# Performance work log

Measured on AMD Instinct MI355X. Metric: run time of the kernel, lower is better.

Reference implementation:

```python
import jax, jax.numpy as jnp
import numpy as np

B, S, D = 4, 8192, 512
WS = 512        # window_size
LB = 1          # look_backward (look_forward = 0, causal)


def setup_inputs() -> dict:
    key = jax.random.key(0)
    k1, k2, k3 = jax.random.split(key, 3)
    text = jax.random.normal(k1, (B, S, D), dtype=jnp.float32)
    audio = jax.random.normal(k2, (B, S, D), dtype=jnp.float32)
    video = jax.random.normal(k3, (B, S, D), dtype=jnp.float32)
    return {"text": text, "audio": audio, "video": video}


def _local_attention(q, k, v, ws=WS, lb=LB):
    # q, k, v: [b, n, d]; sliding-window causal attention, each query window
    # attends to its own window plus `lb` previous windows.
    b, n, d = q.shape
    w = n // ws
    scale = d ** -0.5
    qw = q.reshape(b, w, ws, d) * scale
    kw = k.reshape(b, w, ws, d)
    vw = v.reshape(b, w, ws, d)

    def look_around(x):
        # pad lb windows of zeros at the front, gather lb+1 shifted views
        padded = jnp.pad(x, ((0, 0), (lb, 0), (0, 0), (0, 0)))
        return jnp.concatenate([padded[:, i:i + w] for i in range(lb + 1)], axis=2)

    kk = look_around(kw)  # [b, w, (lb+1)*ws, d]
    vv = look_around(vw)

    # absolute positions for causal + padding mask
    t = jnp.arange(n).reshape(w, ws)                        # query positions [w, ws]
    tk = jnp.pad(t, ((lb, 0), (0, 0)), constant_values=-1)  # pad windows get -1
    bq_k = jnp.concatenate([tk[i:i + w] for i in range(lb + 1)], axis=1)  # [w, (lb+1)*ws]
    mask = (t[:, :, None] >= bq_k[:, None, :]) & (bq_k[:, None, :] >= 0)  # [w, ws, (lb+1)*ws]

    sim = jnp.einsum('bwid,bwjd->bwij', qw, kk)             # [b, w, ws, (lb+1)*ws]
    sim = jnp.where(mask[None], sim, jnp.finfo(sim.dtype).min)
    attn = jax.nn.softmax(sim, axis=-1)
    out = jnp.einsum('bwij,bwjd->bwid', attn, vv)
    return out.reshape(b, n, d)


def reference(text, audio, video):
    # GATSBlock.forward: x = self.local_attn(text, audio, video)
    # i.e. q = text, k = audio, v = video (modalities pre-projected to [b, n, d])
    return _local_attention(text, audio, video)
```

## Files before the change

### kernel.cpp

```cpp
#include <hip/hip_runtime.h>
#include <hip/hip_bf16.h>

#define S_ 8192
#define D_ 512
#define WSZ 512
#define QBLK 128
#define KBLK 32
#define ATT_THREADS 512
#define ATT_LDS (2 * 65536)

using bf16x8 = __attribute__((ext_vector_type(8))) __bf16;
using f32x4  = __attribute__((ext_vector_type(4))) float;

#define GLDS(gp, lp) __builtin_amdgcn_global_load_lds( \
    (const __attribute__((address_space(1))) void*)(gp), \
    (__attribute__((address_space(3))) void*)(lp), 16, 0, 0)

__global__ __launch_bounds__(256) void cvt_k(const float* __restrict__ in,
                                             ushort* __restrict__ out) {
    const int bid = blockIdx.x;
    const int j = bid & 7, t = (bid >> 3) & 255, b = bid >> 11;
    const int u = j * 256 + threadIdx.x;
    const int c = u >> 7, row = (u >> 2) & 31, h = u & 3;
    const float* src = in + ((size_t)(b * S_ + t * 32 + row)) * D_ + c * 32 + h * 8;
    float4 a0 = *(const float4*)(src);
    float4 a1 = *(const float4*)(src + 4);
    bf16x8 o;
    o[0] = (__bf16)a0.x; o[1] = (__bf16)a0.y; o[2] = (__bf16)a0.z; o[3] = (__bf16)a0.w;
    o[4] = (__bf16)a1.x; o[5] = (__bf16)a1.y; o[6] = (__bf16)a1.z; o[7] = (__bf16)a1.w;
    *(bf16x8*)(out + (size_t)(b * 256 + t) * 16384 + u * 8) = o;
}

__global__ __launch_bounds__(256) void tr_v(const float* __restrict__ V,
                                            char* __restrict__ Vt) {
    __shared__ float tile[64][68];
    const int bid = blockIdx.x;
    const int d0 = (bid & 7) * 64;
    const int s0 = ((bid >> 3) & 127) * 64;
    const int b  = bid >> 10;
    const int t  = threadIdx.x;
    {
        const int sl = t >> 2, cg = (t & 3) * 16;
        const float* src = V + ((size_t)b * S_ + s0 + sl) * D_ + d0 + cg;
        #pragma unroll
        for (int j = 0; j < 4; ++j) {
            float4 a = *(const float4*)(src + j * 4);
            *(float4*)&tile[sl][cg + j * 4] = a;
        }
    }
    __syncthreads();
    {
        const int dl = t >> 2, sg = (t & 3) * 16;
        const int d  = d0 + dl;
        const int tt = (s0 + sg) >> 5;
        const int h  = ((s0 + sg) & 31) >> 3;
        bf16x8 o0, o1;
        #pragma unroll
        for (int j = 0; j < 8; ++j) {
            o0[j] = (__bf16)tile[sg + j][dl];
            o1[j] = (__bf16)tile[sg + 8 + j][dl];
        }
        const size_t base = (size_t)(b * 256 + tt) * 32768 +
                            (d >> 4) * 1024 + (d & 15) * 64;
        *(bf16x8*)(Vt + base + h * 16)       = o0;
        *(bf16x8*)(Vt + base + (h + 1) * 16) = o1;
    }
}

__global__ __launch_bounds__(ATT_THREADS, 2) void gats_attn(
    const float* __restrict__ Qg, const char* __restrict__ Kbg,
    const char* __restrict__ Vtg, float* __restrict__ Og)
{
    extern __shared__ char smem[];
    const int tid  = threadIdx.x;
    const int lane = tid & 63;
    const int wv   = tid >> 6;
    const int h    = lane >> 4;
    const int lq   = lane & 15;
    const int laneK = lq * 64 + h * 16;

    const int bid = blockIdx.x;
    const int r2  = bid >> 3;
    const int w   = (bid & 7) * 2 + (r2 & 1);
    const int b   = (r2 >> 1) & 3;
    const int y   = r2 >> 3;
    const int qbase  = w * WSZ + y * QBLK;
    const int wqbase = qbase + wv * 16;

    const float* Qp  = Qg  + (size_t)b * S_ * D_;
    const char*  Kbp = Kbg + (size_t)b * 256 * 32768;
    const char*  Vtp = Vtg + (size_t)b * 256 * 32768;
    float*       Op  = Og  + (size_t)b * S_ * D_;

    const float scale = 0.044194173824159216f;
    const float L2E   = 1.44269504088896f;

    bf16x8 qf[16];
    {
        const int qrow = wqbase + lq;
        const float* qsrc = Qp + (size_t)qrow * D_ + h * 8;
        #pragma unroll
        for (int c = 0; c < 16; ++c) {
            float4 a0 = *(const float4*)(qsrc + c * 32);
            float4 a1 = *(const float4*)(qsrc + c * 32 + 4);
            bf16x8 q;
            q[0] = (__bf16)(a0.x * scale); q[1] = (__bf16)(a0.y * scale);
            q[2] = (__bf16)(a0.z * scale); q[3] = (__bf16)(a0.w * scale);
            q[4] = (__bf16)(a1.x * scale); q[5] = (__bf16)(a1.y * scale);
            q[6] = (__bf16)(a1.z * scale); q[7] = (__bf16)(a1.w * scale);
            qf[c] = q;
        }
    }

    f32x4 acc[32];
    #pragma unroll
    for (int i = 0; i < 32; ++i) acc[i] = (f32x4){0.f, 0.f, 0.f, 0.f};
    float m_run = -1e30f, l_run = 0.f;

    const int kstart = (w == 0) ? 0 : (w - 1) * WSZ;
    const int ktend  = qbase + QBLK;

    auto STAGE = [&](int bufi, int kt) {
        char* kb = smem + bufi * 65536;
        char* vb = kb + 32768;
        const size_t tb = ((size_t)(kt >> 5)) << 15;
        const char* ksrc = Kbp + tb;
        const char* vsrc = Vtp + tb;
        #pragma unroll
        for (int s2 = 0; s2 < 4; ++s2) {
            const int off = wv * 4096 + s2 * 1024;
            GLDS(ksrc + off + lane * 16, kb + off);
            GLDS(vsrc + off + lane * 16, vb + off);
        }
    };

    STAGE(0, kstart);
    int cur = 0;
    for (int kt = kstart; kt < ktend; kt += KBLK) {
        const bool hasnext = (kt + KBLK) < ktend;
        if (hasnext) {
            STAGE(cur ^ 1, kt + KBLK);
            asm volatile("s_waitcnt vmcnt(8)" ::: "memory");
        } else {
            asm volatile("s_waitcnt vmcnt(0)" ::: "memory");
        }
        __builtin_amdgcn_s_barrier();

        if (kt <= wqbase + 15) {
            char* Ksh = smem + cur * 65536;
            char* Vsh = Ksh + 32768;

            f32x4 st[2];
            __builtin_amdgcn_s_setprio(1);
            #pragma unroll
            for (int g = 0; g < 2; ++g) {
                f32x4 sa = (f32x4){0.f, 0.f, 0.f, 0.f};
                f32x4 sb = (f32x4){0.f, 0.f, 0.f, 0.f};
                #pragma unroll
                for (int c = 0; c < 16; ++c) {
                    const int byte = c * 2048 + g * 1024 + laneK;
                    bf16x8 kf = *(const bf16x8*)(Ksh + byte);
                    if (c & 1) sb = __builtin_amdgcn_mfma_f32_16x16x32_bf16(kf, qf[c], sb, 0, 0, 0);
                    else       sa = __builtin_amdgcn_mfma_f32_16x16x32_bf16(kf, qf[c], sa, 0, 0, 0);
                }
                st[g] = sa + sb;
            }
            __builtin_amdgcn_s_setprio(0);

            const int qg = wqbase + lq;
            if (kt + 31 > wqbase) {
                #pragma unroll
                for (int g = 0; g < 2; ++g)
                    #pragma unroll
                    for (int r = 0; r < 4; ++r) {
                        const int key = kt + g * 16 + h * 4 + r;
                        if (key > qg) st[g][r] = -1e30f;
                    }
            }

            float own = st[0][0];
            #pragma unroll
            for (int r = 1; r < 4; ++r) own = fmaxf(own, st[0][r]);
            #pragma unroll
            for (int r = 0; r < 4; ++r) own = fmaxf(own, st[1][r]);
            float tmax = fmaxf(own, __shfl_xor(own, 16));
            tmax = fmaxf(tmax, __shfl_xor(tmax, 32));

            if (__any(tmax > m_run + 8.f)) {
                const float mnew = fmaxf(m_run, tmax);
                const float f = exp2f((m_run - mnew) * L2E);
                m_run = mnew;
                l_run *= f;
                float fr[4];
                #pragma unroll
                for (int r = 0; r < 4; ++r) fr[r] = __shfl(f, h * 4 + r);
                #pragma unroll
                for (int dc = 0; dc < 32; ++dc)
                    #pragma unroll
                    for (int r = 0; r < 4; ++r) acc[dc][r] *= fr[r];
            }

            float p[2][4];
            float rs = 0.f;
            #pragma unroll
            for (int g = 0; g < 2; ++g)
                #pragma unroll
                for (int r = 0; r < 4; ++r) {
                    const float v = exp2f((st[g][r] - m_run) * L2E);
                    p[g][r] = v;
                    rs += v;
                }
            rs += __shfl_xor(rs, 16);
            rs += __shfl_xor(rs, 32);
            l_run += rs;

            uint c0, c1, c2, c3;
            asm("v_cvt_pk_bf16_f32 %0, %1, %2" : "=v"(c0) : "v"(p[0][0]), "v"(p[0][1]));
            asm("v_cvt_pk_bf16_f32 %0, %1, %2" : "=v"(c1) : "v"(p[0][2]), "v"(p[0][3]));
            asm("v_cvt_pk_bf16_f32 %0, %1, %2" : "=v"(c2) : "v"(p[1][0]), "v"(p[1][1]));
            asm("v_cvt_pk_bf16_f32 %0, %1, %2" : "=v"(c3) : "v"(p[1][2]), "v"(p[1][3]));
            const uint x16_0 = __shfl_xor((int)c0, 16), x16_1 = __shfl_xor((int)c1, 16);
            const uint x16_2 = __shfl_xor((int)c2, 16), x16_3 = __shfl_xor((int)c3, 16);
            const uint x32_0 = __shfl_xor((int)c0, 32), x32_1 = __shfl_xor((int)c1, 32);
            const uint x32_2 = __shfl_xor((int)c2, 32), x32_3 = __shfl_xor((int)c3, 32);
            const uint x48_0 = __shfl_xor((int)c0, 48), x48_1 = __shfl_xor((int)c1, 48);
            const uint x48_2 = __shfl_xor((int)c2, 48), x48_3 = __shfl_xor((int)c3, 48);
            union { uint u[4]; bf16x8 v; } pu;
            pu.u[0] = (h == 0) ? c0 : (h == 1) ? x48_0 : (h == 2) ? x32_2 : x16_2;
            pu.u[1] = (h == 0) ? c1 : (h == 1) ? x48_1 : (h == 2) ? x32_3 : x16_3;
            pu.u[2] = (h == 0) ? x16_0 : (h == 1) ? x32_0 : (h == 2) ? x48_2 : c2;
            pu.u[3] = (h == 0) ? x16_1 : (h == 1) ? x32_1 : (h == 2) ? x48_3 : c3;
            const bf16x8 pa = pu.v;

            __builtin_amdgcn_s_setprio(1);
            #pragma unroll
            for (int dc = 0; dc < 32; ++dc) {
                bf16x8 vf = *(const bf16x8*)(Vsh + dc * 1024 + laneK);
                acc[dc] = __builtin_amdgcn_mfma_f32_16x16x32_bf16(pa, vf, acc[dc], 0, 0, 0);
            }
            __builtin_amdgcn_s_setprio(0);
        }
        __builtin_amdgcn_s_barrier();
        cur ^= 1;
    }

    const float invq = 1.0f / l_run;
    float inv[4];
    #pragma unroll
    for (int r = 0; r < 4; ++r) inv[r] = __shfl(invq, h * 4 + r);
    #pragma unroll
    for (int dc = 0; dc < 32; ++dc) {
        #pragma unroll
        for (int r = 0; r < 4; ++r) {
            const int row = wqbase + h * 4 + r;
            const int col = dc * 16 + lq;
            Op[(size_t)row * D_ + col] = acc[dc][r] * inv[r];
        }
    }
}

#define FB_LDS (32768 + 32768 + 4 * 1024)
__global__ __launch_bounds__(256, 2) void gats_attn_fb(
    const float* __restrict__ Qg, const float* __restrict__ Kg,
    const float* __restrict__ Vg, float* __restrict__ Og)
{
    extern __shared__ char smem[];
    char* Ksh = smem;
    char* Vsh = smem + 32768;
    const int tid  = threadIdx.x;
    const int lane = tid & 63;
    const int wv   = tid >> 6;
    char* Psh = smem + 65536 + wv * 1024;
    const int bid = blockIdx.x;
    const int wh  = bid & 7;
    const int r2  = bid >> 3;
    const int w   = wh * 2 + (r2 & 1);
    const int b   = (r2 >> 1) & 3;
    const int y   = r2 >> 3;
    const int qbase  = w * WSZ + y * 64;
    const int wqbase = qbase + wv * 16;
    const size_t boff = (size_t)b * S_ * D_;
    const float* Qp = Qg + boff; const float* Kp = Kg + boff;
    const float* Vp = Vg + boff; float* Op = Og + boff;
    const float scale = 0.044194173824159216f;
    const float L2E   = 1.44269504088896f;
    bf16x8 qf[16];
    {
        const int qrow = wqbase + (lane & 15);
        const float* qsrc = Qp + (size_t)qrow * D_ + ((lane >> 4) * 8);
        #pragma unroll
        for (int c = 0; c < 16; ++c) {
            float4 a0 = *(const float4*)(qsrc + c * 32);
            float4 a1 = *(const float4*)(qsrc + c * 32 + 4);
            bf16x8 q;
            q[0] = (__bf16)(a0.x * scale); q[1] = (__bf16)(a0.y * scale);
            q[2] = (__bf16)(a0.z * scale); q[3] = (__bf16)(a0.w * scale);
            q[4] = (__bf16)(a1.x * scale); q[5] = (__bf16)(a1.y * scale);
            q[6] = (__bf16)(a1.z * scale); q[7] = (__bf16)(a1.w * scale);
            qf[c] = q;
        }
    }
    f32x4 acc[32];
    #pragma unroll
    for (int i = 0; i < 32; ++i) acc[i] = (f32x4){0.f, 0.f, 0.f, 0.f};
    float m_r[4], l_r[4];
    #pragma unroll
    for (int r = 0; r < 4; ++r) { m_r[r] = -1e30f; l_r[r] = 0.f; }
    const int kstart = (w == 0) ? 0 : (w - 1) * WSZ;
    const int ktend  = qbase + 64;
    for (int kt = kstart; kt < ktend; kt += 32) {
        __syncthreads();
        #pragma unroll
        for (int s = 0; s < 8; ++s) {
            const int row = s * 4 + wv;
            const int dof = lane * 8;
            const float4* src = (const float4*)(Kp + (size_t)(kt + row) * D_ + dof);
            float4 a0 = src[0], a1 = src[1];
            bf16x8 kv;
            kv[0] = (__bf16)a0.x; kv[1] = (__bf16)a0.y; kv[2] = (__bf16)a0.z; kv[3] = (__bf16)a0.w;
            kv[4] = (__bf16)a1.x; kv[5] = (__bf16)a1.y; kv[6] = (__bf16)a1.z; kv[7] = (__bf16)a1.w;
            const int byte = row * 1024 + ((dof * 2) ^ ((row & 7) << 4));
            *(bf16x8*)(Ksh + byte) = kv;
        }
        #pragma unroll
        for (int hh = 0; hh < 2; ++hh) {
            const int d = tid + hh * 256;
            #pragma unroll
            for (int it = 0; it < 4; ++it) {
                float vvv[8];
                #pragma unroll
                for (int j = 0; j < 8; ++j)
                    vvv[j] = Vp[(size_t)(kt + it * 8 + j) * D_ + d];
                bf16x8 vb;
                #pragma unroll
                for (int j = 0; j < 8; ++j) vb[j] = (__bf16)vvv[j];
                const int byte = d * 64 + ((it * 16) ^ (((d >> 1) & 3) << 4));
                *(bf16x8*)(Vsh + byte) = vb;
            }
        }
        __syncthreads();
        if (kt > wqbase + 15) continue;
        f32x4 sacc[2];
        #pragma unroll
        for (int g = 0; g < 2; ++g) {
            f32x4 s = (f32x4){0.f, 0.f, 0.f, 0.f};
            const int keyrow = g * 16 + (lane & 15);
            #pragma unroll
            for (int c = 0; c < 16; ++c) {
                const int byte = keyrow * 1024 +
                                 ((c * 64 + (lane >> 4) * 16) ^ ((keyrow & 7) << 4));
                bf16x8 kf = *(const bf16x8*)(Ksh + byte);
                s = __builtin_amdgcn_mfma_f32_16x16x32_bf16(qf[c], kf, s, 0, 0, 0);
            }
            sacc[g] = s;
        }
        #pragma unroll
        for (int g = 0; g < 2; ++g) {
            if (kt + g * 16 + 15 > wqbase) {
                const int kg = kt + g * 16 + (lane & 15);
                #pragma unroll
                for (int r = 0; r < 4; ++r) {
                    const int qrow = wqbase + (lane >> 4) * 4 + r;
                    if (kg > qrow) sacc[g][r] = -1e30f;
                }
            }
        }
        float tmax[4];
        #pragma unroll
        for (int r = 0; r < 4; ++r) {
            float v = fmaxf(sacc[0][r], sacc[1][r]);
            #pragma unroll
            for (int off = 8; off >= 1; off >>= 1)
                v = fmaxf(v, __shfl_xor(v, off));
            tmax[r] = v;
        }
        bool need = false;
        #pragma unroll
        for (int r = 0; r < 4; ++r) need |= (tmax[r] > m_r[r] + 8.f);
        if (__any(need)) {
            #pragma unroll
            for (int r = 0; r < 4; ++r) {
                const float mnew = fmaxf(m_r[r], tmax[r]);
                const float f = exp2f((m_r[r] - mnew) * L2E);
                m_r[r] = mnew; l_r[r] *= f;
                #pragma unroll
                for (int dc = 0; dc < 32; ++dc) acc[dc][r] *= f;
            }
        }
        float rsum[4] = {0.f, 0.f, 0.f, 0.f};
        #pragma unroll
        for (int g = 0; g < 2; ++g) {
            #pragma unroll
            for (int r = 0; r < 4; ++r) {
                const float p = exp2f((sacc[g][r] - m_r[r]) * L2E);
                rsum[r] += p;
                const int prow = (lane >> 4) * 4 + r;
                const int byte = prow * 64 +
                                 ((g * 32 + (lane & 15) * 2) ^ (((prow >> 1) & 3) << 4));
                *(__bf16*)(Psh + byte) = (__bf16)p;
            }
        }
        #pragma unroll
        for (int r = 0; r < 4; ++r) {
            float v = rsum[r];
            #pragma unroll
            for (int off = 8; off >= 1; off >>= 1)
                v += __shfl_xor(v, off);
            l_r[r] += v;
        }
        {
            const int prow  = lane & 15;
            const int pbyte = prow * 64 +
                              (((lane >> 4) * 16) ^ (((prow >> 1) & 3) << 4));
            bf16x8 pa = *(const bf16x8*)(Psh + pbyte);
            #pragma unroll
            for (int dc = 0; dc < 32; ++dc) {
                const int d = dc * 16 + (lane & 15);
                const int vbyte = d * 64 +
                                  (((lane >> 4) * 16) ^ (((d >> 1) & 3) << 4));
                bf16x8 vf = *(const bf16x8*)(Vsh + vbyte);
                acc[dc] = __builtin_amdgcn_mfma_f32_16x16x32_bf16(pa, vf, acc[dc], 0, 0, 0);
            }
        }
    }
    float inv[4];
    #pragma unroll
    for (int r = 0; r < 4; ++r) inv[r] = 1.0f / l_r[r];
    #pragma unroll
    for (int dc = 0; dc < 32; ++dc) {
        #pragma unroll
        for (int r = 0; r < 4; ++r) {
            const int row = wqbase + (lane >> 4) * 4 + r;
            const int col = dc * 16 + (lane & 15);
            Op[(size_t)row * D_ + col] = acc[dc][r] * inv[r];
        }
    }
}

extern "C" void kernel_launch(void* const* d_in, const int* in_sizes, int n_in,
                              void* d_out, int out_size, void* d_ws, size_t ws_size,
                              hipStream_t stream) {
    const float* q = (const float*)d_in[0];
    const float* k = (const float*)d_in[1];
    const float* v = (const float*)d_in[2];
    float* o = (float*)d_out;

    const size_t elems = (size_t)4 * S_ * D_ * 4;
    const size_t need  = elems * 2 * 2;
    if (ws_size >= need) {
        char* kb = (char*)d_ws;
        char* vt = (char*)d_ws + elems * 2;
        cvt_k<<<dim3(8192), dim3(256), 0, stream>>>(k, (ushort*)kb);
        tr_v <<<dim3(4096), dim3(256), 0, stream>>>(v, vt);
        hipFuncSetAttribute((const void*)gats_attn,
                            hipFuncAttributeMaxDynamicSharedMemorySize, ATT_LDS);
        gats_attn<<<dim3(256), dim3(ATT_THREADS), ATT_LDS, stream>>>(q, kb, vt, o);
    } else {
        hipFuncSetAttribute((const void*)gats_attn_fb,
                            hipFuncAttributeMaxDynamicSharedMemorySize, FB_LDS);
        gats_attn_fb<<<dim3(512), dim3(256), FB_LDS, stream>>>(q, k, v, o);
    }
}
```

Before: 158.6 us.

## Pair waves to share P via LDS and use 32x32x16 MFMA for PV

```diff
diff --git a/kernel.cpp b/kernel.cpp
--- a/kernel.cpp
+++ b/kernel.cpp
@@ -7,10 +7,13 @@
 #define QBLK 128
 #define KBLK 32
 #define ATT_THREADS 512
-#define ATT_LDS (2 * 65536)
+#define PREG 131072
+#define PSTRIDE 2560
+#define ATT_LDS (PREG + 4 * PSTRIDE)
 
 using bf16x8 = __attribute__((ext_vector_type(8))) __bf16;
 using f32x4  = __attribute__((ext_vector_type(4))) float;
+using f32x16 = __attribute__((ext_vector_type(16))) float;
 
 #define GLDS(gp, lp) __builtin_amdgcn_global_load_lds( \
     (const __attribute__((address_space(1))) void*)(gp), \
@@ -43,27 +46,25 @@
         const int sl = t >> 2, cg = (t & 3) * 16;
         const float* src = V + ((size_t)b * S_ + s0 + sl) * D_ + d0 + cg;
         #pragma unroll
-        for (int j = 0; j < 4; ++j) {
-            float4 a = *(const float4*)(src + j * 4);
-            *(float4*)&tile[sl][cg + j * 4] = a;
-        }
+        for (int j = 0; j < 4; ++j)
+            *(float4*)&tile[sl][cg + j * 4] = *(const float4*)(src + j * 4);
     }
     __syncthreads();
     {
         const int dl = t >> 2, sg = (t & 3) * 16;
         const int d  = d0 + dl;
         const int tt = (s0 + sg) >> 5;
-        const int h  = ((s0 + sg) & 31) >> 3;
+        const int kk = (s0 + sg) & 31;
         bf16x8 o0, o1;
         #pragma unroll
         for (int j = 0; j < 8; ++j) {
             o0[j] = (__bf16)tile[sg + j][dl];
             o1[j] = (__bf16)tile[sg + 8 + j][dl];
         }
-        const size_t base = (size_t)(b * 256 + tt) * 32768 +
-                            (d >> 4) * 1024 + (d & 15) * 64;
-        *(bf16x8*)(Vt + base + h * 16)       = o0;
-        *(bf16x8*)(Vt + base + (h + 1) * 16) = o1;
+        char* base = Vt + (size_t)(b * 256 + tt) * 32768 +
+                     (d >> 5) * 2048 + (d & 31) * 16;
+        *(bf16x8*)(base + (kk >> 4) * 1024)       = o0;
+        *(bf16x8*)(base + (kk >> 4) * 1024 + 512) = o1;
     }
 }
 
@@ -77,6 +78,12 @@
     const int wv   = tid >> 6;
     const int h    = lane >> 4;
     const int lq   = lane & 15;
+    const int hh   = lane >> 5;
+    const int l31  = lane & 31;
+    const int u    = wv & 1;
+    const int pr   = wv >> 1;
+    char* Pp = smem + PREG + pr * PSTRIDE;
+    char* Pf = Pp + 2048;
     const int laneK = lq * 64 + h * 16;
 
     const int bid = blockIdx.x;
@@ -84,8 +91,9 @@
     const int w   = (bid & 7) * 2 + (r2 & 1);
     const int b   = (r2 >> 1) & 3;
     const int y   = r2 >> 3;
-    const int qbase  = w * WSZ + y * QBLK;
-    const int wqbase = qbase + wv * 16;
+    const int qbase    = w * WSZ + y * QBLK;
+    const int pairbase = qbase + pr * 32;
+    const int wqbase   = qbase + wv * 16;
 
     const float* Qp  = Qg  + (size_t)b * S_ * D_;
     const char*  Kbp = Kbg + (size_t)b * 256 * 32768;
@@ -112,9 +120,11 @@
         }
     }
 
-    f32x4 acc[32];
-    #pragma unroll
-    for (int i = 0; i < 32; ++i) acc[i] = (f32x4){0.f, 0.f, 0.f, 0.f};
+    f32x16 acc[8];
+    #pragma unroll
+    for (int dt = 0; dt < 8; ++dt)
+        #pragma unroll
+        for (int rg = 0; rg < 16; ++rg) acc[dt][rg] = 0.f;
     float m_run = -1e30f, l_run = 0.f;
 
     const int kstart = (w == 0) ? 0 : (w - 1) * WSZ;
@@ -146,10 +156,11 @@
         }
         __builtin_amdgcn_s_barrier();
 
-        if (kt <= wqbase + 15) {
-            char* Ksh = smem + cur * 65536;
-            char* Vsh = Ksh + 32768;
-
+        const bool active = (kt <= pairbase + 31);
+        char* Ksh = smem + cur * 65536;
+        char* Vsh = Ksh + 32768;
+
+        if (active) {
             f32x4 st[2];
             __builtin_amdgcn_s_setprio(1);
             #pragma unroll
@@ -178,65 +189,75 @@
                     }
             }
 
-            float own = st[0][0];
-            #pragma unroll
-            for (int r = 1; r < 4; ++r) own = fmaxf(own, st[0][r]);
-            #pragma unroll
-            for (int r = 0; r < 4; ++r) own = fmaxf(own, st[1][r]);
+            float own = fmaxf(fmaxf(fmaxf(st[0][0], st[0][1]), fmaxf(st[0][2], st[0][3])),
+                              fmaxf(fmaxf(st[1][0], st[1][1]), fmaxf(st[1][2], st[1][3])));
             float tmax = fmaxf(own, __shfl_xor(own, 16));
             tmax = fmaxf(tmax, __shfl_xor(tmax, 32));
 
-            if (__any(tmax > m_run + 8.f)) {
+            const bool anyneed = __any(tmax > m_run + 8.f);
+            float f_val = 1.0f;
+            if (anyneed) {
                 const float mnew = fmaxf(m_run, tmax);
-                const float f = exp2f((m_run - mnew) * L2E);
+                f_val = exp2f((m_run - mnew) * L2E);
                 m_run = mnew;
-                l_run *= f;
-                float fr[4];
-                #pragma unroll
-                for (int r = 0; r < 4; ++r) fr[r] = __shfl(f, h * 4 + r);
-                #pragma unroll
-                for (int dc = 0; dc < 32; ++dc)
-                    #pragma unroll
-                    for (int r = 0; r < 4; ++r) acc[dc][r] *= fr[r];
-            }
-
-            float p[2][4];
-            float rs = 0.f;
-            #pragma unroll
-            for (int g = 0; g < 2; ++g)
-                #pragma unroll
-                for (int r = 0; r < 4; ++r) {
-                    const float v = exp2f((st[g][r] - m_run) * L2E);
-                    p[g][r] = v;
-                    rs += v;
-                }
+                l_run *= f_val;
+            }
+
+            const float p00 = exp2f((st[0][0] - m_run) * L2E);
+            const float p01 = exp2f((st[0][1] - m_run) * L2E);
+            const float p02 = exp2f((st[0][2] - m_run) * L2E);
+            const float p03 = exp2f((st[0][3] - m_run) * L2E);
+            const float p10 = exp2f((st[1][0] - m_run) * L2E);
+            const float p11 = exp2f((st[1][1] - m_run) * L2E);
+            const float p12 = exp2f((st[1][2] - m_run) * L2E);
+            const float p13 = exp2f((st[1][3] - m_run) * L2E);
+            float rs = p00 + p01 + p02 + p03 + p10 + p11 + p12 + p13;
             rs += __shfl_xor(rs, 16);
             rs += __shfl_xor(rs, 32);
             l_run += rs;
 
             uint c0, c1, c2, c3;
-            asm("v_cvt_pk_bf16_f32 %0, %1, %2" : "=v"(c0) : "v"(p[0][0]), "v"(p[0][1]));
-            asm("v_cvt_pk_bf16_f32 %0, %1, %2" : "=v"(c1) : "v"(p[0][2]), "v"(p[0][3]));
-            asm("v_cvt_pk_bf16_f32 %0, %1, %2" : "=v"(c2) : "v"(p[1][0]), "v"(p[1][1]));
-            asm("v_cvt_pk_bf16_f32 %0, %1, %2" : "=v"(c3) : "v"(p[1][2]), "v"(p[1][3]));
-            const uint x16_0 = __shfl_xor((int)c0, 16), x16_1 = __shfl_xor((int)c1, 16);
-            const uint x16_2 = __shfl_xor((int)c2, 16), x16_3 = __shfl_xor((int)c3, 16);
-            const uint x32_0 = __shfl_xor((int)c0, 32), x32_1 = __shfl_xor((int)c1, 32);
-            const uint x32_2 = __shfl_xor((int)c2, 32), x32_3 = __shfl_xor((int)c3, 32);
-            const uint x48_0 = __shfl_xor((int)c0, 48), x48_1 = __shfl_xor((int)c1, 48);
-            const uint x48_2 = __shfl_xor((int)c2, 48), x48_3 = __shfl_xor((int)c3, 48);
-            union { uint u[4]; bf16x8 v; } pu;
-            pu.u[0] = (h == 0) ? c0 : (h == 1) ? x48_0 : (h == 2) ? x32_2 : x16_2;
-            pu.u[1] = (h == 0) ? c1 : (h == 1) ? x48_1 : (h == 2) ? x32_3 : x16_3;
-            pu.u[2] = (h == 0) ? x16_0 : (h == 1) ? x32_0 : (h == 2) ? x48_2 : c2;
-            pu.u[3] = (h == 0) ? x16_1 : (h == 1) ? x32_1 : (h == 2) ? x48_3 : c3;
-            const bf16x8 pa = pu.v;
-
+            asm("v_cvt_pk_bf16_f32 %0, %1, %2" : "=v"(c0) : "v"(p00), "v"(p01));
+            asm("v_cvt_pk_bf16_f32 %0, %1, %2" : "=v"(c1) : "v"(p02), "v"(p03));
+            asm("v_cvt_pk_bf16_f32 %0, %1, %2" : "=v"(c2) : "v"(p10), "v"(p11));
+            asm("v_cvt_pk_bf16_f32 %0, %1, %2" : "=v"(c3) : "v"(p12), "v"(p13));
+            const int wbase = (h >> 1) * 512 + (h & 1) * 8 + (u * 16 + lq) * 16;
+            *(uint*)(Pp + wbase)            = c0;
+            *(uint*)(Pp + wbase + 4)        = c1;
+            *(uint*)(Pp + 1024 + wbase)     = c2;
+            *(uint*)(Pp + 1024 + wbase + 4) = c3;
+            if (h == 0)    *(float*)(Pf + (u * 16 + lq) * 4) = f_val;
+            if (lane == 0) *(uint*)(Pf + 128 + u * 4) = anyneed ? 1u : 0u;
+        }
+
+        asm volatile("s_waitcnt lgkmcnt(0)" ::: "memory");
+        __builtin_amdgcn_sched_barrier(0);
+        __builtin_amdgcn_s_barrier();
+
+        if (active) {
+            const uint2 fl = *(const uint2*)(Pf + 128);
+            if (fl.x | fl.y) {
+                f32x4 fr[4];
+                #pragma unroll
+                for (int i = 0; i < 4; ++i)
+                    fr[i] = *(const f32x4*)(Pf + i * 32 + hh * 16);
+                #pragma unroll
+                for (int dt = 0; dt < 8; ++dt)
+                    #pragma unroll
+                    for (int rg = 0; rg < 16; ++rg)
+                        acc[dt][rg] *= fr[rg >> 2][rg & 3];
+            }
+
+            bf16x8 pa0 = *(const bf16x8*)(Pp + hh * 512 + l31 * 16);
+            bf16x8 pa1 = *(const bf16x8*)(Pp + 1024 + hh * 512 + l31 * 16);
             __builtin_amdgcn_s_setprio(1);
             #pragma unroll
-            for (int dc = 0; dc < 32; ++dc) {
-                bf16x8 vf = *(const bf16x8*)(Vsh + dc * 1024 + laneK);
-                acc[dc] = __builtin_amdgcn_mfma_f32_16x16x32_bf16(pa, vf, acc[dc], 0, 0, 0);
+            for (int dt = 0; dt < 8; ++dt) {
+                const int vb = (u * 8 + dt) * 2048 + hh * 512 + l31 * 16;
+                bf16x8 v0 = *(const bf16x8*)(Vsh + vb);
+                bf16x8 v1 = *(const bf16x8*)(Vsh + vb + 1024);
+                acc[dt] = __builtin_amdgcn_mfma_f32_32x32x16_bf16(pa0, v0, acc[dt], 0, 0, 0);
+                acc[dt] = __builtin_amdgcn_mfma_f32_32x32x16_bf16(pa1, v1, acc[dt], 0, 0, 0);
             }
             __builtin_amdgcn_s_setprio(0);
         }
@@ -244,17 +265,23 @@
         cur ^= 1;
     }
 
-    const float invq = 1.0f / l_run;
-    float inv[4];
-    #pragma unroll
-    for (int r = 0; r < 4; ++r) inv[r] = __shfl(invq, h * 4 + r);
-    #pragma unroll
-    for (int dc = 0; dc < 32; ++dc) {
-        #pragma unroll
-        for (int r = 0; r < 4; ++r) {
-            const int row = wqbase + h * 4 + r;
-            const int col = dc * 16 + lq;
-            Op[(size_t)row * D_ + col] = acc[dc][r] * inv[r];
+    if (h == 0) *(float*)(Pf + (u * 16 + lq) * 4) = l_run;
+    asm volatile("s_waitcnt lgkmcnt(0)" ::: "memory");
+    __builtin_amdgcn_s_barrier();
+    f32x4 iv[4];
+    #pragma unroll
+    for (int i = 0; i < 4; ++i) {
+        f32x4 lv = *(const f32x4*)(Pf + i * 32 + hh * 16);
+        iv[i][0] = 1.0f / lv[0]; iv[i][1] = 1.0f / lv[1];
+        iv[i][2] = 1.0f / lv[2]; iv[i][3] = 1.0f / lv[3];
+    }
+    #pragma unroll
+    for (int dt = 0; dt < 8; ++dt) {
+        const int colb = u * 256 + dt * 32 + l31;
+        #pragma unroll
+        for (int rg = 0; rg < 16; ++rg) {
+            const int row = pairbase + (rg & 3) + 8 * (rg >> 2) + 4 * hh;
+            Op[(size_t)row * D_ + colb] = acc[dt][rg] * iv[rg >> 2][rg & 3];
         }
     }
 }
@@ -323,8 +350,8 @@
             *(bf16x8*)(Ksh + byte) = kv;
         }
         #pragma unroll
-        for (int hh = 0; hh < 2; ++hh) {
-            const int d = tid + hh * 256;
+        for (int hh2 = 0; hh2 < 2; ++hh2) {
+            const int d = tid + hh2 * 256;
             #pragma unroll
             for (int it = 0; it < 4; ++it) {
                 float vvv[8];
```

Measured after the change: 147.2 us. -7.2%, faster.
